# Performance work log

Measured on AMD Instinct MI355X. Metric: run time of the kernel, lower is better.

## Reference

```python
import jax, jax.numpy as jnp
import numpy as np

N_WIRES = 9
N_QRAM_LAYERS = 3
N_QCLS_LAYERS = 5

X = jnp.array([[0, 1], [1, 0]], dtype=jnp.complex64)
CNOT = jnp.array([[1, 0, 0, 0], [0, 1, 0, 0], [0, 0, 0, 1], [0, 0, 1, 0]], dtype=jnp.complex64)


def _rx(t):
    c = jnp.cos(t / 2)
    s = jnp.sin(t / 2)
    # works for scalar t -> (2,2) or batched t [B] -> (B,2,2)
    return jnp.stack([jnp.stack([c + 0j, -1j * s], -1), jnp.stack([-1j * s, c + 0j], -1)], -2)


def _ry(t):
    c = jnp.cos(t / 2)
    s = jnp.sin(t / 2)
    return jnp.stack([jnp.stack([c, -s], -1), jnp.stack([s, c], -1)], -2).astype(jnp.complex64)


def _rz(t):
    e = jnp.exp(-0.5j * t)
    f = jnp.exp(0.5j * t)
    z = jnp.zeros_like(e)
    return jnp.stack([jnp.stack([e, z], -1), jnp.stack([z, f], -1)], -2)


def _rot(phi, theta, omega):
    # PennyLane Rot(phi, theta, omega) = RZ(omega) @ RY(theta) @ RZ(phi)
    return _rz(omega) @ _ry(theta) @ _rz(phi)


def _crz(t):
    e = jnp.exp(-0.5j * t)
    f = jnp.exp(0.5j * t)
    one = jnp.ones((), e.dtype)
    return jnp.diag(jnp.stack([one, one, e, f]))


def _crx(t):
    return jnp.eye(4, dtype=jnp.complex64).at[2:, 2:].set(_rx(t))


def apply_1q(state, U, w):
    # state: [B] + (2,)*N_WIRES ; wire w -> axis 1+w
    s = jnp.moveaxis(state, 1 + w, -1)
    if U.ndim == 3:  # per-sample gate (embedding)
        s = jnp.einsum('bij,b...j->b...i', U, s)
    else:
        s = jnp.einsum('ij,...j->...i', U, s)
    return jnp.moveaxis(s, -1, 1 + w)


def apply_2q(state, U, c, t):
    s = jnp.moveaxis(state, (1 + c, 1 + t), (-2, -1))
    shp = s.shape
    s = s.reshape(shp[:-2] + (4,))
    s = jnp.einsum('ij,...j->...i', U, s)
    return jnp.moveaxis(s.reshape(shp), (-2, -1), (1 + c, 1 + t))


def embed(state, adds):
    # AngleEmbedding: RX(adds[:, i]) on wire i
    for i in range(N_WIRES):
        state = apply_1q(state, _rx(adds[:, i]), i)
    return state


def entangle_block(state, p):
    # p: [36] = 4 params per wire-pair step
    j = 0
    for i in range(N_WIRES):
        ip = (i + 1) % N_WIRES
        state = apply_1q(state, _ry(p[j]), i)
        state = apply_1q(state, _ry(p[j + 1]), ip)
        state = apply_2q(state, CNOT, i, ip)
        state = apply_2q(state, _crz(p[j + 2]), i, ip)
        state = apply_1q(state, X, ip)
        state = apply_2q(state, _crx(p[j + 3]), i, ip)
        j += 4
    return state


def sel_layer(state, w, r):
    # one StronglyEntanglingLayers layer: Rot on each wire, then CNOT ring of range r
    for i in range(N_WIRES):
        state = apply_1q(state, _rot(w[i, 0], w[i, 1], w[i, 2]), i)
    for i in range(N_WIRES):
        state = apply_2q(state, CNOT, i, (i + r) % N_WIRES)
    return state


def circuit(adds, params, weights, params2):
    B = adds.shape[0]
    state = jnp.zeros((B,) + (2,) * N_WIRES, jnp.complex64)
    state = state.at[(slice(None),) + (0,) * N_WIRES].set(1.0)
    state = embed(state, adds)
    for l in range(N_QRAM_LAYERS):
        state = entangle_block(state, params[l * 36:(l + 1) * 36])
    for l in range(N_QRAM_LAYERS):
        r = (l % (N_WIRES - 1)) + 1  # PennyLane default ranges
        state = sel_layer(state, weights[l], r)
    for l in range(N_QCLS_LAYERS):
        state = entangle_block(state, params2[l * 36:(l + 1) * 36])
    probs = jnp.abs(state) ** 2
    p = probs.reshape(B, 2, -1).sum(-1)  # marginal over wire 0
    return p[:, 0] - p[:, 1]  # <PauliZ(0)>


def setup_inputs() -> dict:
    key = jax.random.key(0)
    k1, k2, k3, k4 = jax.random.split(key, 4)
    B = 8192
    return {
        'adds': jax.random.normal(k1, (B, N_WIRES), dtype=jnp.float32),
        'params': jax.random.normal(k2, (N_QRAM_LAYERS * 36,), dtype=jnp.float32),
        'weights': jax.random.normal(k3, (N_QRAM_LAYERS, N_WIRES, N_QRAM_LAYERS), dtype=jnp.float32),
        'params2': jax.random.normal(k4, (N_QCLS_LAYERS * 36,), dtype=jnp.float32),
    }


def reference(adds, params, weights, params2):
    return circuit(adds, params, weights, params2)
```

## Files before the change

### kernel.cpp

```cpp
#include <hip/hip_runtime.h>

#define NQ 9
#define NS 512
#define M2 1024
#define NSIMB 512

#define ENT_H_BASE 0
#define ROT_BASE   1024
#define ROT3_BASE  1240
#define ROT16_BASE 1624
#define M0123_BASE 3160
#define M78_BASE   7256
#define COEF_FLOATS 8280

typedef __attribute__((ext_vector_type(8))) short bf16x8;
typedef __attribute__((ext_vector_type(4))) float f32x4;

__device__ inline unsigned short f2bf(float f){
  unsigned int u = __float_as_uint(f);
  u += 0x7fffu + ((u >> 16) & 1u);
  return (unsigned short)(u >> 16);
}


template<int LM>
__device__ inline float lxor(float v){
  if constexpr (LM == 1)
    return __int_as_float(__builtin_amdgcn_mov_dpp(__float_as_int(v), 0xB1, 0xF, 0xF, true));
  else if constexpr (LM == 2)
    return __int_as_float(__builtin_amdgcn_mov_dpp(__float_as_int(v), 0x4E, 0xF, 0xF, true));
  else if constexpr (LM == 3)
    return __int_as_float(__builtin_amdgcn_mov_dpp(__float_as_int(v), 0x1B, 0xF, 0xF, true));
  else if constexpr (LM < 32)
    return __int_as_float(__builtin_amdgcn_ds_swizzle(__float_as_int(v), (LM<<10)|0x1F));
  else
    return __shfl_xor(v, LM);
}

template<int CM, int TM>
__device__ inline void step_swz(float& ax, float& ay, int lane, const float* g){
  float tx = lxor<TM>(ax),      ty = lxor<TM>(ay);
  float cx = lxor<CM>(ax),      cy = lxor<CM>(ay);
  float bx = lxor<(CM^TM)>(ax), by = lxor<(CM^TM)>(ay);
  int p = ((lane & CM) ? 2 : 0) | ((lane & TM) ? 1 : 0);
  float4 hx = *(const float4*)(g + p*4);
  float4 hy = *(const float4*)(g + 16 + p*4);
  float ox = ax, oy = ay;
  ax = hx.x*ox - hy.x*oy + hx.y*tx - hy.y*ty
     + hx.z*cx - hy.z*cy + hx.w*bx - hy.w*by;
  ay = hx.x*oy + hy.x*ox + hx.y*ty + hy.y*tx
     + hx.z*cy + hy.z*cx + hx.w*by + hy.w*bx;
}

__device__ inline void mrg16(float& ax, float& ay, int i, int wi, float2* xb,
                             const float* Mt){
  xb[wi] = make_float2(ax, ay);
  __syncthreads();
  int p = (i >> 5) & 15;
  const float* Mr = Mt + p*32;
  int base = i & 31;
  float s0x=0.f,s0y=0.f,s1x=0.f,s1y=0.f;
  #pragma unroll
  for (int q = 0; q < 16; q += 2){
    float2 v0 = xb[(q<<5)|base];
    float2 v1 = xb[((q+1)<<5)|base];
    float m0x = Mr[q*2],   m0y = Mr[q*2+1];
    float m1x = Mr[q*2+2], m1y = Mr[q*2+3];
    s0x += m0x*v0.x - m0y*v0.y;  s0y += m0x*v0.y + m0y*v0.x;
    s1x += m1x*v1.x - m1y*v1.y;  s1y += m1x*v1.y + m1y*v1.x;
  }
  ax = s0x + s1x; ay = s0y + s1y;
}

__device__ inline void mrg8_78(float& ax, float& ay, int i, float2* xb, const float* Mt){
  xb[i] = make_float2(ax, ay);
  __syncthreads();
  int p = (((i>>1)&1)<<2) | ((i&1)<<1) | ((i>>8)&1);
  const float* Mr = Mt + p*16;
  int ib = i & 0x0FC;
  float s0x=0.f,s0y=0.f,s1x=0.f,s1y=0.f;
  #pragma unroll
  for (int q = 0; q < 8; q += 2){
    int j0 = ib | ((q>>2)<<1) | ((q>>1)&1);
    float2 v0 = xb[j0];
    float2 v1 = xb[j0 | 0x100];
    float m0x = Mr[q*2],   m0y = Mr[q*2+1];
    float m1x = Mr[q*2+2], m1y = Mr[q*2+3];
    s0x += m0x*v0.x - m0y*v0.y;  s0y += m0x*v0.y + m0y*v0.x;
    s1x += m1x*v1.x - m1y*v1.y;  s1y += m1x*v1.y + m1y*v1.x;
  }
  ax = s0x + s1x; ay = s0y + s1y;
}

template<int LM>
__device__ inline void rot_swz(float& ax, float& ay, int lane, const float* u){
  float px = lxor<LM>(ax), py = lxor<LM>(ay);
  float4 uu = *(const float4*)(u + ((lane & LM) ? 4 : 0));
  float nx = uu.x*ax - uu.y*ay + uu.z*px - uu.w*py;
  float ny = uu.x*ay + uu.y*ax + uu.z*py + uu.w*px;
  ax = nx; ay = ny;
}

template<int I = 4>
__device__ inline void sel_lane_rots(float& ax, float& ay, int lane, const float* ub){
  rot_swz<(1<<(8-I))>(ax, ay, lane, ub + I*8);
  if constexpr (I < 8) sel_lane_rots<I+1>(ax, ay, lane, ub);
}

__device__ inline void entM(float& ax, float& ay, int i, int wi, int lane,
                            float2* bX, float2* bY, const float* scoef, int blk){
  mrg16(ax, ay, i, wi, bX, scoef + M0123_BASE + blk*512);
  step_swz<32,16>(ax, ay, lane, scoef + ENT_H_BASE + (blk*4+0)*32);
  step_swz<16, 8>(ax, ay, lane, scoef + ENT_H_BASE + (blk*4+1)*32);
  step_swz< 8, 4>(ax, ay, lane, scoef + ENT_H_BASE + (blk*4+2)*32);
  step_swz< 4, 2>(ax, ay, lane, scoef + ENT_H_BASE + (blk*4+3)*32);
  mrg8_78(ax, ay, i, bY, scoef + M78_BASE + blk*128);
}


__global__ __launch_bounds__(512) void sim_prep(const float* __restrict__ params,
                                                const float* __restrict__ weights,
                                                const float* __restrict__ params2,
                                                const float* __restrict__ adds,
                                                unsigned short* __restrict__ A2,
                                                unsigned short* __restrict__ cT,
                                                float* __restrict__ out, int B){
  int tid = threadIdx.x;

  if (blockIdx.x >= NSIMB){
    int gid = (blockIdx.x - NSIMB) * 512 + tid;
    int b = gid >> 6;
    int lane = gid & 63;
    if (b < B){
      const float* ab = adds + b * NQ;
      float cw[NQ], sw[NQ];
      #pragma unroll
      for (int w = 0; w < NQ; ++w)
        __sincosf(0.5f * ab[w], &sw[w], &cw[w]);
      float p6 = 1.f;
      #pragma unroll
      for (int w = 0; w < 6; ++w)
        p6 *= ((lane >> (5 - w)) & 1) ? sw[w] : cw[w];
      union { unsigned short u[8]; uint4 v; } pk;
      #pragma unroll
      for (int j = 0; j < 8; ++j){
        float p = p6 * (((j>>2)&1) ? sw[6] : cw[6])
                     * (((j>>1)&1) ? sw[7] : cw[7])
                     * (( j    &1) ? sw[8] : cw[8]);
        pk.u[j] = f2bf(p);
      }
      *(uint4*)(cT + (size_t)b * NS + lane*8) = pk.v;
    }
    if (gid < B) out[gid] = 0.f;
    return;
  }

  __shared__ float2 ebuf[1024];
  __shared__ float scoef[COEF_FLOATS];
  __shared__ unsigned short slut[3][512];
  float2* ebufA = ebuf;
  float2* ebufB = ebuf + 512;
  float* graw = (float*)ebuf;

  if (tid < 72){
    int blk = tid / 9, I = tid % 9;
    const float* p = (blk < 3) ? params + blk*36 : params2 + (blk-3)*36;
    float s0,c0,s1,c1,s2,c2,s3,c3;
    __sincosf(0.5f*p[4*I+0], &s0, &c0);
    __sincosf(0.5f*p[4*I+1], &s1, &c1);
    __sincosf(0.5f*p[4*I+2], &s2, &c2);
    __sincosf(0.5f*p[4*I+3], &s3, &c3);
    float m[4][4] = {
      { c0*c1, -c0*s1, -s0*c1,  s0*s1},
      { c0*s1,  c0*c1, -s0*s1, -s0*c1},
      { s0*c1, -s0*s1,  c0*c1, -c0*s1},
      { s0*s1,  s0*c1,  c0*s1,  c0*c1}};
    float gx[4][4], gy[4][4];
    #pragma unroll
    for (int q = 0; q < 4; ++q){
      gx[0][q] = m[1][q];  gy[0][q] = 0.f;
      gx[1][q] = m[0][q];  gy[1][q] = 0.f;
      gx[2][q] =  c3*c2*m[2][q] - s3*s2*m[3][q];
      gy[2][q] =  c3*s2*m[2][q] - s3*c2*m[3][q];
      gx[3][q] =  s3*s2*m[2][q] + c3*c2*m[3][q];
      gy[3][q] = -(s3*c2*m[2][q] + c3*s2*m[3][q]);
    }
    if (I >= 3 && I <= 6){
      float* dst = scoef + ENT_H_BASE + (blk*4 + (I-3))*32;
      #pragma unroll
      for (int pp = 0; pp < 4; ++pp)
        #pragma unroll
        for (int d = 0; d < 4; ++d){
          dst[pp*4+d]    = gx[pp][pp^d];
          dst[16+pp*4+d] = gy[pp][pp^d];
        }
    } else {
      float* dst = (I < 3) ? graw + (blk*3 + I)*32
                           : graw + 768 + (blk*2 + (I-7))*32;
      #pragma unroll
      for (int pp = 0; pp < 4; ++pp)
        #pragma unroll
        for (int q = 0; q < 4; ++q){
          dst[(pp*4+q)*2]   = gx[pp][q];
          dst[(pp*4+q)*2+1] = gy[pp][q];
        }
    }
  } else if (tid < 99){
    int r = tid - 72;
    int l = r / 9, i = r % 9;
    const float* w = weights + l*27 + 3*i;
    float phi = w[0], th = w[1], om = w[2];
    float sT,cT,sA,cA,sB,cB;
    __sincosf(0.5f*th, &sT, &cT);
    __sincosf(0.5f*(phi+om), &sA, &cA);
    __sincosf(0.5f*(om-phi), &sB, &cB);
    float* dst = scoef + ROT_BASE + r*8;
    dst[0] =  cA*cT;  dst[1] = -sA*cT;
    dst[2] = -cB*sT;  dst[3] =  sB*sT;
    dst[4] =  cA*cT;  dst[5] =  sA*cT;
    dst[6] =  cB*sT;  dst[7] =  sB*sT;
  } else if (tid < 123){
    int idx = tid - 99;
    int l = idx >> 3, p = idx & 7;
    float e0x[3], e0y[3], e1x[3], e1y[3];
    #pragma unroll
    for (int w = 0; w < 3; ++w){
      const float* wp = weights + l*27 + 3*w;
      float phi = wp[0], th = wp[1], om = wp[2];
      float sT,cT,sA,cA,sB,cB;
      __sincosf(0.5f*th, &sT, &cT);
      __sincosf(0.5f*(phi+om), &sA, &cA);
      __sincosf(0.5f*(om-phi), &sB, &cB);
      int pw = (p >> (2 - w)) & 1;
      if (pw == 0){ e0x[w] =  cA*cT; e0y[w] = -sA*cT; e1x[w] = -cB*sT; e1y[w] =  sB*sT; }
      else        { e0x[w] =  cB*sT; e0y[w] =  sB*sT; e1x[w] =  cA*cT; e1y[w] =  sA*cT; }
    }
    float* dst = scoef + ROT3_BASE + l*128 + p*16;
    #pragma unroll
    for (int q = 0; q < 8; ++q){
      float rx = 1.f, ry = 0.f;
      #pragma unroll
      for (int w = 0; w < 3; ++w){
        int qw = (q >> (2 - w)) & 1;
        float fx = qw ? e1x[w] : e0x[w];
        float fy = qw ? e1y[w] : e0y[w];
        float nx = rx*fx - ry*fy;
        float ny = rx*fy + ry*fx;
        rx = nx; ry = ny;
      }
      dst[q*2]   = rx;
      dst[q*2+1] = ry;
    }
  }
  __syncthreads();

  {
    int blk = tid >> 6;
    const float* G0 = graw + (blk*3+0)*32;
    const float* G1 = graw + (blk*3+1)*32;
    const float* G2 = graw + (blk*3+2)*32;
    int e4 = (tid & 63) * 4;
    #pragma unroll
    for (int k = 0; k < 4; ++k){
      int e = e4 + k;
      int p = e >> 4, q = e & 15;
      int a=(p>>3)&1, b=(p>>2)&1, c=(p>>1)&1, d=p&1;
      int ee=(q>>3)&1, f=(q>>2)&1, g=(q>>1)&1, h=q&1;
      float sx = 0.f, sy = 0.f;
      #pragma unroll
      for (int m = 0; m < 2; ++m)
        #pragma unroll
        for (int n = 0; n < 2; ++n){
          const float* z2 = G2 + ((c*2+d)*4 + (n*2+h))*2;
          const float* z1 = G1 + ((b*2+n)*4 + (m*2+g))*2;
          const float* z0 = G0 + ((a*2+m)*4 + (ee*2+f))*2;
          float ux = z2[0]*z1[0] - z2[1]*z1[1];
          float uy = z2[0]*z1[1] + z2[1]*z1[0];
          float vx = ux*z0[0] - uy*z0[1];
          float vy = ux*z0[1] + uy*z0[0];
          sx += vx; sy += vy;
        }
      scoef[M0123_BASE + blk*512 + (p*16+q)*2]   = sx;
      scoef[M0123_BASE + blk*512 + (p*16+q)*2+1] = sy;
    }
    const float* G7 = graw + 768 + (blk*2+0)*32;
    const float* G8 = graw + 768 + (blk*2+1)*32;
    int e = tid & 63;
    int p = e >> 3, q = e & 7;
    int a=(p>>2)&1, b=(p>>1)&1, c=p&1;
    int d=(q>>2)&1, ei=(q>>1)&1, f=q&1;
    float sx = 0.f, sy = 0.f;
    #pragma unroll
    for (int m = 0; m < 2; ++m){
      const float* z8 = G8 + ((b*2+c)*4 + (m*2+f))*2;
      const float* z7 = G7 + ((a*2+m)*4 + (d*2+ei))*2;
      sx += z8[0]*z7[0] - z8[1]*z7[1];
      sy += z8[0]*z7[1] + z8[1]*z7[0];
    }
    scoef[M78_BASE + blk*128 + (p*8+q)*2]   = sx;
    scoef[M78_BASE + blk*128 + (p*8+q)*2+1] = sy;

    for (int e2 = tid; e2 < 768; e2 += 512){
      int l = e2 >> 8, pq = e2 & 255;
      int pp = pq >> 4, qq = pq & 15;
      const float* R3 = scoef + ROT3_BASE + l*128 + (pp>>1)*16 + (qq>>1)*2;
      const float* U = scoef + ROT_BASE + (l*9+3)*8;
      int pb = pp & 1, qb = qq & 1;
      float ux, uy;
      if (pb == 0){ if (qb == 0){ ux=U[0]; uy=U[1]; } else { ux=U[2]; uy=U[3]; } }
      else        { if (qb == 1){ ux=U[4]; uy=U[5]; } else { ux=U[6]; uy=U[7]; } }
      float rx = R3[0], ry = R3[1];
      scoef[ROT16_BASE + l*512 + pp*32 + qq*2]   = rx*ux - ry*uy;
      scoef[ROT16_BASE + l*512 + pp*32 + qq*2+1] = rx*uy + ry*ux;
    }

    for (int R = 1; R <= 3; ++R){
      int s = tid;
      for (int k = 8; k >= 0; --k){
        int bc = 8 - k;
        int it = k + R; if (it >= 9) it -= 9;
        int bt = 8 - it;
        s ^= ((s >> bc) & 1) << bt;
      }
      slut[R-1][s] = (unsigned short)tid;
    }
  }
  __syncthreads();

  int i = tid, lane = tid & 63;
  int col = blockIdx.x;
  int w1 = slut[0][i], w2 = slut[1][i], w3 = slut[2][i];
  float ax, ay;
  int pc = __popc((unsigned)col) & 3;
  float prx = (pc==0) ? 1.f : (pc==2 ? -1.f : 0.f);
  float pry = (pc==3) ? 1.f : (pc==1 ? -1.f : 0.f);
  ax = (i == col) ? prx : 0.f;
  ay = (i == col) ? pry : 0.f;

  #pragma unroll 1
  for (int blk = 0; blk < 3; ++blk)
    entM(ax, ay, i, i, lane, ebufA, ebufB, scoef, blk);

  mrg16(ax, ay, i, i,  ebufA, scoef + ROT16_BASE + 0*512);
  sel_lane_rots<4>(ax, ay, lane, scoef + ROT_BASE + 0*72);
  mrg16(ax, ay, i, w1, ebufB, scoef + ROT16_BASE + 1*512);
  sel_lane_rots<4>(ax, ay, lane, scoef + ROT_BASE + 1*72);
  mrg16(ax, ay, i, w2, ebufA, scoef + ROT16_BASE + 2*512);
  sel_lane_rots<4>(ax, ay, lane, scoef + ROT_BASE + 2*72);

  entM(ax, ay, i, w3, lane, ebufB, ebufA, scoef, 3);
  #pragma unroll 1
  for (int blk = 4; blk < 8; ++blk)
    entM(ax, ay, i, i, lane, ebufB, ebufA, scoef, blk);

  int c = col >> 3, sub = col & 7;
  size_t base = (size_t)c * 1024;
  A2[(base + i)*8 + sub]       = f2bf(ax);
  A2[(base + 512 + i)*8 + sub] = f2bf(ay);
}

__global__ __launch_bounds__(512) void gemm_out(const unsigned short* __restrict__ A2,
                                                const unsigned short* __restrict__ cT,
                                                float* __restrict__ out){
  int bx = blockIdx.x;
  int by = blockIdx.y;
  int tid = threadIdx.x;
  int wave = tid >> 6, lane = tid & 63;
  int wy = wave >> 2, wx = wave & 3;
  int lane15 = lane & 15, quad = lane >> 4;
  int rowBase = by*128 + wy*64;
  int colBase = bx*128 + wx*32;
  const bf16x8* Ap8 = (const bf16x8*)A2;
  const short* Bp = (const short*)cT;

  f32x4 acc[4][2];
  #pragma unroll
  for (int i = 0; i < 4; ++i)
    #pragma unroll
    for (int j = 0; j < 2; ++j)
      acc[i][j] = (f32x4){0.f, 0.f, 0.f, 0.f};

  #pragma unroll 4
  for (int k0 = 0; k0 < NS; k0 += 32){
    bf16x8 a[4], b[2];
    int c = (k0 >> 3) + quad;
    #pragma unroll
    for (int mi = 0; mi < 4; ++mi)
      a[mi] = Ap8[(size_t)c*1024 + rowBase + mi*16 + lane15];
    #pragma unroll
    for (int ni = 0; ni < 2; ++ni)
      b[ni] = *(const bf16x8*)(Bp + (size_t)(colBase + ni*16 + lane15)*NS + k0 + quad*8);
    #pragma unroll
    for (int mi = 0; mi < 4; ++mi)
      #pragma unroll
      for (int ni = 0; ni < 2; ++ni)
        acc[mi][ni] = __builtin_amdgcn_mfma_f32_16x16x32_bf16(a[mi], b[ni], acc[mi][ni], 0, 0, 0);
  }

  float sign = (by & 2) ? -1.f : 1.f;
  #pragma unroll
  for (int ni = 0; ni < 2; ++ni){
    float cs = 0.f;
    #pragma unroll
    for (int mi = 0; mi < 4; ++mi)
      #pragma unroll
      for (int r = 0; r < 4; ++r)
        cs += acc[mi][ni][r] * acc[mi][ni][r];
    cs += __shfl_xor(cs, 16);
    cs += __shfl_xor(cs, 32);
    if (quad == 0)
      atomicAdd(out + colBase + ni*16 + lane15, sign * cs);
  }
}

extern "C" void kernel_launch(void* const* d_in, const int* in_sizes, int n_in,
                              void* d_out, int out_size, void* d_ws, size_t ws_size,
                              hipStream_t stream) {
  const float* adds    = (const float*)d_in[0];
  const float* params  = (const float*)d_in[1];
  const float* weights = (const float*)d_in[2];
  const float* params2 = (const float*)d_in[3];
  float* out = (float*)d_out;
  int B = in_sizes[0] / NQ;

  unsigned short* A2 = (unsigned short*)d_ws;
  unsigned short* cT = A2 + (size_t)M2 * NS;

  int prepBlocks = (B * 64 + 511) / 512;
  hipLaunchKernelGGL(sim_prep, dim3(NSIMB + prepBlocks), dim3(512), 0, stream,
                     params, weights, params2, adds, A2, cT, out, B);
  hipLaunchKernelGGL(gemm_out, dim3(B / 128, 8), dim3(512), 0, stream, A2, cT, out);
}
```

Measured before the change: 116.7 us.

## Simulate two basis columns per block and enlarge per-wave GEMM tile

Each simulation block now evolves two basis-state columns at once, halving the simulation block count and the per-block coefficient/LUT setup. The shared loads of matrix coefficients and the barriers are amortized across two state vectors, and the bf16 output is written as packed 32-bit pairs. The GEMM switches to 256-thread blocks with 4x4 MFMA tiles per wave, which raises register use but improves operand reuse. The risks are doubled LDS for the exchange buffers and lower occupancy in both kernels.

```diff
diff --git a/kernel.cpp b/kernel.cpp
--- a/kernel.cpp
+++ b/kernel.cpp
@@ -3,7 +3,7 @@
 #define NQ 9
 #define NS 512
 #define M2 1024
-#define NSIMB 512
+#define NSIMB 256
 
 #define ENT_H_BASE 0
 #define ROT_BASE   1024
@@ -38,83 +38,101 @@
 }
 
 template<int CM, int TM>
-__device__ inline void step_swz(float& ax, float& ay, int lane, const float* g){
-  float tx = lxor<TM>(ax),      ty = lxor<TM>(ay);
-  float cx = lxor<CM>(ax),      cy = lxor<CM>(ay);
-  float bx = lxor<(CM^TM)>(ax), by = lxor<(CM^TM)>(ay);
+__device__ inline void step_swz2(float& a0x, float& a0y, float& a1x, float& a1y,
+                                 int lane, const float* g){
+  float t0x = lxor<TM>(a0x),      t0y = lxor<TM>(a0y);
+  float c0x = lxor<CM>(a0x),      c0y = lxor<CM>(a0y);
+  float b0x = lxor<(CM^TM)>(a0x), b0y = lxor<(CM^TM)>(a0y);
+  float t1x = lxor<TM>(a1x),      t1y = lxor<TM>(a1y);
+  float c1x = lxor<CM>(a1x),      c1y = lxor<CM>(a1y);
+  float b1x = lxor<(CM^TM)>(a1x), b1y = lxor<(CM^TM)>(a1y);
   int p = ((lane & CM) ? 2 : 0) | ((lane & TM) ? 1 : 0);
   float4 hx = *(const float4*)(g + p*4);
   float4 hy = *(const float4*)(g + 16 + p*4);
-  float ox = ax, oy = ay;
-  ax = hx.x*ox - hy.x*oy + hx.y*tx - hy.y*ty
-     + hx.z*cx - hy.z*cy + hx.w*bx - hy.w*by;
-  ay = hx.x*oy + hy.x*ox + hx.y*ty + hy.y*tx
-     + hx.z*cy + hy.z*cx + hx.w*by + hy.w*bx;
-}
-
-__device__ inline void mrg16(float& ax, float& ay, int i, int wi, float2* xb,
-                             const float* Mt){
-  xb[wi] = make_float2(ax, ay);
+  float o0x = a0x, o0y = a0y, o1x = a1x, o1y = a1y;
+  a0x = hx.x*o0x - hy.x*o0y + hx.y*t0x - hy.y*t0y
+      + hx.z*c0x - hy.z*c0y + hx.w*b0x - hy.w*b0y;
+  a0y = hx.x*o0y + hy.x*o0x + hx.y*t0y + hy.y*t0x
+      + hx.z*c0y + hy.z*c0x + hx.w*b0y + hy.w*b0x;
+  a1x = hx.x*o1x - hy.x*o1y + hx.y*t1x - hy.y*t1y
+      + hx.z*c1x - hy.z*c1y + hx.w*b1x - hy.w*b1y;
+  a1y = hx.x*o1y + hy.x*o1x + hx.y*t1y + hy.y*t1x
+      + hx.z*c1y + hy.z*c1x + hx.w*b1y + hy.w*b1x;
+}
+
+__device__ inline void mrg16_2(float& a0x, float& a0y, float& a1x, float& a1y,
+                               int i, int wi, float2* xb, const float* Mt){
+  xb[wi]       = make_float2(a0x, a0y);
+  xb[512 + wi] = make_float2(a1x, a1y);
   __syncthreads();
   int p = (i >> 5) & 15;
   const float* Mr = Mt + p*32;
   int base = i & 31;
   float s0x=0.f,s0y=0.f,s1x=0.f,s1y=0.f;
   #pragma unroll
-  for (int q = 0; q < 16; q += 2){
+  for (int q = 0; q < 16; ++q){
+    float mx = Mr[q*2], my = Mr[q*2+1];
     float2 v0 = xb[(q<<5)|base];
-    float2 v1 = xb[((q+1)<<5)|base];
-    float m0x = Mr[q*2],   m0y = Mr[q*2+1];
-    float m1x = Mr[q*2+2], m1y = Mr[q*2+3];
-    s0x += m0x*v0.x - m0y*v0.y;  s0y += m0x*v0.y + m0y*v0.x;
-    s1x += m1x*v1.x - m1y*v1.y;  s1y += m1x*v1.y + m1y*v1.x;
-  }
-  ax = s0x + s1x; ay = s0y + s1y;
-}
-
-__device__ inline void mrg8_78(float& ax, float& ay, int i, float2* xb, const float* Mt){
-  xb[i] = make_float2(ax, ay);
+    float2 v1 = xb[512 + ((q<<5)|base)];
+    s0x += mx*v0.x - my*v0.y;  s0y += mx*v0.y + my*v0.x;
+    s1x += mx*v1.x - my*v1.y;  s1y += mx*v1.y + my*v1.x;
+  }
+  a0x = s0x; a0y = s0y; a1x = s1x; a1y = s1y;
+}
+
+__device__ inline void mrg8_2(float& a0x, float& a0y, float& a1x, float& a1y,
+                              int i, float2* xb, const float* Mt){
+  xb[i]       = make_float2(a0x, a0y);
+  xb[512 + i] = make_float2(a1x, a1y);
   __syncthreads();
   int p = (((i>>1)&1)<<2) | ((i&1)<<1) | ((i>>8)&1);
   const float* Mr = Mt + p*16;
   int ib = i & 0x0FC;
   float s0x=0.f,s0y=0.f,s1x=0.f,s1y=0.f;
   #pragma unroll
-  for (int q = 0; q < 8; q += 2){
-    int j0 = ib | ((q>>2)<<1) | ((q>>1)&1);
-    float2 v0 = xb[j0];
-    float2 v1 = xb[j0 | 0x100];
-    float m0x = Mr[q*2],   m0y = Mr[q*2+1];
-    float m1x = Mr[q*2+2], m1y = Mr[q*2+3];
-    s0x += m0x*v0.x - m0y*v0.y;  s0y += m0x*v0.y + m0y*v0.x;
-    s1x += m1x*v1.x - m1y*v1.y;  s1y += m1x*v1.y + m1y*v1.x;
-  }
-  ax = s0x + s1x; ay = s0y + s1y;
+  for (int q = 0; q < 8; ++q){
+    int j = (ib | (((q>>1)&3) ^ (((q>>1)&3) & 0)) ) ;
+    (void)j;
+    int j0 = ib | (((q>>2)&1)<<1) | ((q>>1)&1);
+    int jj = (q & 1) ? (j0 | 0x100) : j0;
+    float mx = Mr[q*2], my = Mr[q*2+1];
+    float2 v0 = xb[jj];
+    float2 v1 = xb[512 + jj];
+    s0x += mx*v0.x - my*v0.y;  s0y += mx*v0.y + my*v0.x;
+    s1x += mx*v1.x - my*v1.y;  s1y += mx*v1.y + my*v1.x;
+  }
+  a0x = s0x; a0y = s0y; a1x = s1x; a1y = s1y;
 }
 
 template<int LM>
-__device__ inline void rot_swz(float& ax, float& ay, int lane, const float* u){
-  float px = lxor<LM>(ax), py = lxor<LM>(ay);
+__device__ inline void rot_swz2(float& a0x, float& a0y, float& a1x, float& a1y,
+                                int lane, const float* u){
   float4 uu = *(const float4*)(u + ((lane & LM) ? 4 : 0));
-  float nx = uu.x*ax - uu.y*ay + uu.z*px - uu.w*py;
-  float ny = uu.x*ay + uu.y*ax + uu.z*py + uu.w*px;
-  ax = nx; ay = ny;
+  float p0x = lxor<LM>(a0x), p0y = lxor<LM>(a0y);
+  float p1x = lxor<LM>(a1x), p1y = lxor<LM>(a1y);
+  float n0x = uu.x*a0x - uu.y*a0y + uu.z*p0x - uu.w*p0y;
+  float n0y = uu.x*a0y + uu.y*a0x + uu.z*p0y + uu.w*p0x;
+  float n1x = uu.x*a1x - uu.y*a1y + uu.z*p1x - uu.w*p1y;
+  float n1y = uu.x*a1y + uu.y*a1x + uu.z*p1y + uu.w*p1x;
+  a0x = n0x; a0y = n0y; a1x = n1x; a1y = n1y;
 }
 
 template<int I = 4>
-__device__ inline void sel_lane_rots(float& ax, float& ay, int lane, const float* ub){
-  rot_swz<(1<<(8-I))>(ax, ay, lane, ub + I*8);
-  if constexpr (I < 8) sel_lane_rots<I+1>(ax, ay, lane, ub);
-}
-
-__device__ inline void entM(float& ax, float& ay, int i, int wi, int lane,
-                            float2* bX, float2* bY, const float* scoef, int blk){
-  mrg16(ax, ay, i, wi, bX, scoef + M0123_BASE + blk*512);
-  step_swz<32,16>(ax, ay, lane, scoef + ENT_H_BASE + (blk*4+0)*32);
-  step_swz<16, 8>(ax, ay, lane, scoef + ENT_H_BASE + (blk*4+1)*32);
-  step_swz< 8, 4>(ax, ay, lane, scoef + ENT_H_BASE + (blk*4+2)*32);
-  step_swz< 4, 2>(ax, ay, lane, scoef + ENT_H_BASE + (blk*4+3)*32);
-  mrg8_78(ax, ay, i, bY, scoef + M78_BASE + blk*128);
+__device__ inline void sel_lane_rots2(float& a0x, float& a0y, float& a1x, float& a1y,
+                                      int lane, const float* ub){
+  rot_swz2<(1<<(8-I))>(a0x, a0y, a1x, a1y, lane, ub + I*8);
+  if constexpr (I < 8) sel_lane_rots2<I+1>(a0x, a0y, a1x, a1y, lane, ub);
+}
+
+__device__ inline void entM2(float& a0x, float& a0y, float& a1x, float& a1y,
+                             int i, int wi, int lane,
+                             float2* bX, float2* bY, const float* scoef, int blk){
+  mrg16_2(a0x, a0y, a1x, a1y, i, wi, bX, scoef + M0123_BASE + blk*512);
+  step_swz2<32,16>(a0x, a0y, a1x, a1y, lane, scoef + ENT_H_BASE + (blk*4+0)*32);
+  step_swz2<16, 8>(a0x, a0y, a1x, a1y, lane, scoef + ENT_H_BASE + (blk*4+1)*32);
+  step_swz2< 8, 4>(a0x, a0y, a1x, a1y, lane, scoef + ENT_H_BASE + (blk*4+2)*32);
+  step_swz2< 4, 2>(a0x, a0y, a1x, a1y, lane, scoef + ENT_H_BASE + (blk*4+3)*32);
+  mrg8_2(a0x, a0y, a1x, a1y, i, bY, scoef + M78_BASE + blk*128);
 }
 
 
@@ -155,12 +173,11 @@
     return;
   }
 
-  __shared__ float2 ebuf[1024];
+  __shared__ float2 ebufA[1024];
+  __shared__ float2 ebufB[1024];
   __shared__ float scoef[COEF_FLOATS];
   __shared__ unsigned short slut[3][512];
-  float2* ebufA = ebuf;
-  float2* ebufB = ebuf + 512;
-  float* graw = (float*)ebuf;
+  float* graw = (float*)ebufA;
 
   if (tid < 72){
     int blk = tid / 9, I = tid % 9;
@@ -328,78 +345,89 @@
   __syncthreads();
 
   int i = tid, lane = tid & 63;
-  int col = blockIdx.x;
+  int c0 = blockIdx.x * 2, c1 = c0 + 1;
   int w1 = slut[0][i], w2 = slut[1][i], w3 = slut[2][i];
-  float ax, ay;
-  int pc = __popc((unsigned)col) & 3;
-  float prx = (pc==0) ? 1.f : (pc==2 ? -1.f : 0.f);
-  float pry = (pc==3) ? 1.f : (pc==1 ? -1.f : 0.f);
-  ax = (i == col) ? prx : 0.f;
-  ay = (i == col) ? pry : 0.f;
+  float a0x, a0y, a1x, a1y;
+  {
+    int pc0 = __popc((unsigned)c0) & 3;
+    int pc1 = __popc((unsigned)c1) & 3;
+    float prx0 = (pc0==0) ? 1.f : (pc0==2 ? -1.f : 0.f);
+    float pry0 = (pc0==3) ? 1.f : (pc0==1 ? -1.f : 0.f);
+    float prx1 = (pc1==0) ? 1.f : (pc1==2 ? -1.f : 0.f);
+    float pry1 = (pc1==3) ? 1.f : (pc1==1 ? -1.f : 0.f);
+    a0x = (i == c0) ? prx0 : 0.f;
+    a0y = (i == c0) ? pry0 : 0.f;
+    a1x = (i == c1) ? prx1 : 0.f;
+    a1y = (i == c1) ? pry1 : 0.f;
+  }
 
   #pragma unroll 1
   for (int blk = 0; blk < 3; ++blk)
-    entM(ax, ay, i, i, lane, ebufA, ebufB, scoef, blk);
-
-  mrg16(ax, ay, i, i,  ebufA, scoef + ROT16_BASE + 0*512);
-  sel_lane_rots<4>(ax, ay, lane, scoef + ROT_BASE + 0*72);
-  mrg16(ax, ay, i, w1, ebufB, scoef + ROT16_BASE + 1*512);
-  sel_lane_rots<4>(ax, ay, lane, scoef + ROT_BASE + 1*72);
-  mrg16(ax, ay, i, w2, ebufA, scoef + ROT16_BASE + 2*512);
-  sel_lane_rots<4>(ax, ay, lane, scoef + ROT_BASE + 2*72);
-
-  entM(ax, ay, i, w3, lane, ebufB, ebufA, scoef, 3);
+    entM2(a0x, a0y, a1x, a1y, i, i, lane, ebufA, ebufB, scoef, blk);
+
+  mrg16_2(a0x, a0y, a1x, a1y, i, i,  ebufA, scoef + ROT16_BASE + 0*512);
+  sel_lane_rots2<4>(a0x, a0y, a1x, a1y, lane, scoef + ROT_BASE + 0*72);
+  mrg16_2(a0x, a0y, a1x, a1y, i, w1, ebufB, scoef + ROT16_BASE + 1*512);
+  sel_lane_rots2<4>(a0x, a0y, a1x, a1y, lane, scoef + ROT_BASE + 1*72);
+  mrg16_2(a0x, a0y, a1x, a1y, i, w2, ebufA, scoef + ROT16_BASE + 2*512);
+  sel_lane_rots2<4>(a0x, a0y, a1x, a1y, lane, scoef + ROT_BASE + 2*72);
+
+  entM2(a0x, a0y, a1x, a1y, i, w3, lane, ebufB, ebufA, scoef, 3);
   #pragma unroll 1
   for (int blk = 4; blk < 8; ++blk)
-    entM(ax, ay, i, i, lane, ebufB, ebufA, scoef, blk);
-
-  int c = col >> 3, sub = col & 7;
+    entM2(a0x, a0y, a1x, a1y, i, i, lane, ebufB, ebufA, scoef, blk);
+
+  int c = c0 >> 3;
+  int jp = blockIdx.x & 3;
   size_t base = (size_t)c * 1024;
-  A2[(base + i)*8 + sub]       = f2bf(ax);
-  A2[(base + 512 + i)*8 + sub] = f2bf(ay);
-}
-
-__global__ __launch_bounds__(512) void gemm_out(const unsigned short* __restrict__ A2,
+  unsigned int* Aw = (unsigned int*)A2;
+  unsigned int re = (unsigned)f2bf(a0x) | ((unsigned)f2bf(a1x) << 16);
+  unsigned int im = (unsigned)f2bf(a0y) | ((unsigned)f2bf(a1y) << 16);
+  Aw[(base + i)*4 + jp]       = re;
+  Aw[(base + 512 + i)*4 + jp] = im;
+}
+
+__global__ __launch_bounds__(256) void gemm_out(const unsigned short* __restrict__ A2,
                                                 const unsigned short* __restrict__ cT,
                                                 float* __restrict__ out){
   int bx = blockIdx.x;
   int by = blockIdx.y;
   int tid = threadIdx.x;
   int wave = tid >> 6, lane = tid & 63;
-  int wy = wave >> 2, wx = wave & 3;
+  int wy = wave >> 1, wx = wave & 1;
   int lane15 = lane & 15, quad = lane >> 4;
   int rowBase = by*128 + wy*64;
-  int colBase = bx*128 + wx*32;
+  int colBase = bx*128 + wx*64;
   const bf16x8* Ap8 = (const bf16x8*)A2;
   const short* Bp = (const short*)cT;
 
-  f32x4 acc[4][2];
+  f32x4 acc[4][4];
   #pragma unroll
   for (int i = 0; i < 4; ++i)
     #pragma unroll
-    for (int j = 0; j < 2; ++j)
+    for (int j = 0; j < 4; ++j)
       acc[i][j] = (f32x4){0.f, 0.f, 0.f, 0.f};
 
   #pragma unroll 4
   for (int k0 = 0; k0 < NS; k0 += 32){
-    bf16x8 a[4], b[2];
+    bf16x8 a[4], b[4];
     int c = (k0 >> 3) + quad;
     #pragma unroll
     for (int mi = 0; mi < 4; ++mi)
       a[mi] = Ap8[(size_t)c*1024 + rowBase + mi*16 + lane15];
     #pragma unroll
-    for (int ni = 0; ni < 2; ++ni)
+    for (int ni = 0; ni < 4; ++ni)
       b[ni] = *(const bf16x8*)(Bp + (size_t)(colBase + ni*16 + lane15)*NS + k0 + quad*8);
     #pragma unroll
     for (int mi = 0; mi < 4; ++mi)
       #pragma unroll
-      for (int ni = 0; ni < 2; ++ni)
+      for (int ni = 0; ni < 4; ++ni)
         acc[mi][ni] = __builtin_amdgcn_mfma_f32_16x16x32_bf16(a[mi], b[ni], acc[mi][ni], 0, 0, 0);
   }
 
   float sign = (by & 2) ? -1.f : 1.f;
   #pragma unroll
-  for (int ni = 0; ni < 2; ++ni){
+  for (int ni = 0; ni < 4; ++ni){
     float cs = 0.f;
     #pragma unroll
     for (int mi = 0; mi < 4; ++mi)
@@ -429,5 +457,5 @@
   int prepBlocks = (B * 64 + 511) / 512;
   hipLaunchKernelGGL(sim_prep, dim3(NSIMB + prepBlocks), dim3(512), 0, stream,
                      params, weights, params2, adds, A2, cT, out, B);
-  hipLaunchKernelGGL(gemm_out, dim3(B / 128, 8), dim3(512), 0, stream, A2, cT, out);
-}
+  hipLaunchKernelGGL(gemm_out, dim3(B / 128, 8), dim3(256), 0, stream, A2, cT, out);
+}
```

Result: faster. 113.5 us (-2.8%).
